# Optimization experiments

Measured on AMD Instinct MI355X. Metric: run time of the kernel, lower is better.

## Reference

```python
import jax, jax.numpy as jnp
import numpy as np

NUM_HEADS = 12


def setup_inputs() -> dict:
    key = jax.random.key(0)
    k1, k2, k3 = jax.random.split(key, 3)
    B, F, P, D = 8, 16, 196, 768
    x = jax.random.normal(k1, (B, F, P, D), dtype=jnp.float32)
    w_qkv = jax.random.normal(k2, (3 * D, D), dtype=jnp.float32) * (D ** -0.5)
    w_proj = jax.random.normal(k3, (D, D), dtype=jnp.float32) * (D ** -0.5)
    b_proj = jnp.zeros((D,), dtype=jnp.float32)
    return {"x": x, "w_qkv": w_qkv, "w_proj": w_proj, "b_proj": b_proj}


def reference(x, w_qkv, w_proj, b_proj):
    B, F, P, D = x.shape
    H = NUM_HEADS
    hd = D // H
    H2 = H // 2
    scale = hd ** -0.5
    N = F * P

    xf = x.reshape(B, N, D)
    qkv = jnp.einsum('bnd,ed->bne', xf, w_qkv)              # (B, N, 3D)
    qkv = qkv.reshape(B, N, 3, H, hd).transpose(2, 0, 3, 1, 4)
    q, k, v = qkv[0], qkv[1], qkv[2]                         # (B, H, N, hd)

    # split heads: first half spatial, second half temporal
    qs, qt = q[:, :H2], q[:, H2:]
    ks, kt = k[:, :H2], k[:, H2:]
    vs, vt = v[:, :H2], v[:, H2:]

    # spatial attention over patches within each frame
    qs = qs.reshape(B * F, H2, P, hd)
    ks = ks.reshape(B * F, H2, P, hd)
    vs = vs.reshape(B * F, H2, P, hd)
    attn_s = jax.nn.softmax(jnp.einsum('nhqd,nhkd->nhqk', qs, ks) * scale, axis=-1)
    ws = jnp.einsum('nhqk,nhkd->nhqd', attn_s, vs)           # (B*F, H2, P, hd)

    # temporal attention: raw row-major reshape, faithful to torch .reshape
    qt = qt.reshape(B * P, H2, F, hd)
    kt = kt.reshape(B * P, H2, F, hd)
    vt = vt.reshape(B * P, H2, F, hd)
    attn_t = jax.nn.softmax(jnp.einsum('mhqd,mhkd->mhqk', qt, kt) * scale, axis=-1)
    wt = jnp.einsum('mhqk,mhkd->mhqd', attn_t, vt)           # (B*P, H2, F, hd)

    ws = ws.reshape(B, H2, N, hd)
    wt = wt.reshape(B, H2, N, hd)
    w = jnp.concatenate([ws, wt], axis=1)                    # (B, H, N, hd)
    w = w.transpose(0, 2, 1, 3).reshape(B, N, D)

    out = jnp.einsum('bnd,ed->bne', w, w_proj) + b_proj
    return out.reshape(B, F, P, D)
```

## Files before the change

### kernel.cpp

```cpp
#include <hip/hip_runtime.h>

#define DEV __device__ __forceinline__

typedef _Float16 half8  __attribute__((ext_vector_type(8)));
typedef _Float16 half4h __attribute__((ext_vector_type(4)));
typedef float    f32x4  __attribute__((ext_vector_type(4)));

static constexpr int Bb = 8;
static constexpr int Ff = 16;
static constexpr int Pp = 196;
static constexpr int Dd = 768;
static constexpr int Hh = 12;
static constexpr int HD = 64;
static constexpr int Nn = 3136;
static constexpr int NC = 392;

#define MFMA(a, b, c) __builtin_amdgcn_mfma_f32_16x16x32_f16(a, b, c, 0, 0, 0)

DEV void gll16(const _Float16* g, _Float16* l) {
  __builtin_amdgcn_global_load_lds(
      (__attribute__((address_space(1))) void*)(g),
      (__attribute__((address_space(3))) void*)(l), 16, 0, 0);
}

DEV void lds_fence() { asm volatile("s_waitcnt lgkmcnt(0)" ::: "memory"); }

__global__ __launch_bounds__(256) void cvt_all(const float* __restrict__ x,
                                               const float* __restrict__ wq,
                                               const float* __restrict__ wp,
                                               _Float16* __restrict__ xh,
                                               _Float16* __restrict__ wqh,
                                               _Float16* __restrict__ wph) {
  const int NX = 4816896, NQ = 442368;
  int i = blockIdx.x * 256 + threadIdx.x;
  const float* s;
  _Float16* d;
  int j;
  if (i < NX) { s = x; d = xh; j = i; }
  else if (i < NX + NQ) { s = wq; d = wqh; j = i - NX; }
  else { s = wp; d = wph; j = i - NX - NQ; }
  f32x4 v = ((const f32x4*)s)[j];
  half4h h;
  h.x = (_Float16)v.x; h.y = (_Float16)v.y;
  h.z = (_Float16)v.z; h.w = (_Float16)v.w;
  ((half4h*)d)[j] = h;
}

__global__ __launch_bounds__(256) void gemm_qkv(const _Float16* __restrict__ X,
                                                const _Float16* __restrict__ W,
                                                _Float16* __restrict__ Q8,
                                                _Float16* __restrict__ K8,
                                                _Float16* __restrict__ V8) {
  __shared__ __align__(16) _Float16 smem[128 * 132];
  _Float16* As = smem;
  _Float16* Bs = smem + 128 * 32;
  const int tid = threadIdx.x;
  const int lane = tid & 63, wid = tid >> 6;
  const int l15 = lane & 15, quad = lane >> 4;
  const int row0 = blockIdx.y * 128;
  const int e0 = blockIdx.x * 128;
  const int wm = (wid >> 1) * 64, wn = (wid & 1) * 64;

  const _Float16* Ag = X + (size_t)row0 * Dd;
  const _Float16* Bg = W + (size_t)e0 * Dd;

  f32x4 acc[4][4];
#pragma unroll
  for (int i = 0; i < 4; ++i)
#pragma unroll
    for (int j = 0; j < 4; ++j) acc[i][j] = (f32x4)0.0f;

  const int c0 = tid, c1 = tid + 256;
  const int r0s = c0 >> 2, o0 = ((c0 & 3) ^ ((r0s >> 1) & 3)) * 8;
  const int r1s = c1 >> 2, o1 = ((c1 & 3) ^ ((r1s >> 1) & 3)) * 8;
  const int csel = ((quad ^ ((l15 >> 1) & 3))) * 8;

  for (int kt = 0; kt < 24; ++kt) {
    const int k0 = kt * 32;
    __syncthreads();
    gll16(Ag + (size_t)r0s * Dd + k0 + o0, As + c0 * 8);
    gll16(Bg + (size_t)r0s * Dd + k0 + o0, Bs + c0 * 8);
    gll16(Ag + (size_t)r1s * Dd + k0 + o1, As + c1 * 8);
    gll16(Bg + (size_t)r1s * Dd + k0 + o1, Bs + c1 * 8);
    __syncthreads();
    half8 af[4], bf[4];
#pragma unroll
    for (int t = 0; t < 4; ++t) {
      af[t] = *(const half8*)(As + (wm + t * 16 + l15) * 32 + csel);
      bf[t] = *(const half8*)(Bs + (wn + t * 16 + l15) * 32 + csel);
    }
#pragma unroll
    for (int i = 0; i < 4; ++i)
#pragma unroll
      for (int j = 0; j < 4; ++j) acc[i][j] = MFMA(af[i], bf[j], acc[i][j]);
  }

  __syncthreads();
  const int tsel = e0 / Dd;
  if (tsel == 2) {
#pragma unroll
    for (int i = 0; i < 4; ++i)
#pragma unroll
      for (int j = 0; j < 4; ++j) {
        const int m = wm + i * 16 + quad * 4;
        const int n = wn + j * 16 + l15;
        half4h hv;
        hv.x = (_Float16)acc[i][j].x; hv.y = (_Float16)acc[i][j].y;
        hv.z = (_Float16)acc[i][j].z; hv.w = (_Float16)acc[i][j].w;
        *(half4h*)(smem + n * 132 + m) = hv;
      }
    __syncthreads();
    for (int c = tid; c < 2048; c += 256) {
      const int ncl = c >> 7, el = c & 127;
      const int e = e0 + el;
      const int h = (e >> 6) % Hh, d = e & 63;
      const int r = row0 + ncl * 8;
      const int b = r / Nn, n = r % Nn;
      const half4h lo = *(const half4h*)(smem + el * 132 + ncl * 8);
      const half4h hi = *(const half4h*)(smem + el * 132 + ncl * 8 + 4);
      half8 v;
#pragma unroll
      for (int z = 0; z < 4; ++z) { v[z] = lo[z]; v[4 + z] = hi[z]; }
      *(half8*)(V8 + (((size_t)(b * Hh + h) * NC + (n >> 3)) * 64 + d) * 8) = v;
    }
  } else {
    _Float16* Ob = (tsel == 0) ? Q8 : K8;
#pragma unroll
    for (int i = 0; i < 4; ++i)
#pragma unroll
      for (int j = 0; j < 4; ++j) {
        const int n = wn + j * 16 + l15;
#pragma unroll
        for (int r = 0; r < 4; ++r) {
          const int m = wm + i * 16 + quad * 4 + r;
          smem[m * 132 + n] = (_Float16)acc[i][j][r];
        }
      }
    __syncthreads();
    for (int c = tid; c < 2048; c += 256) {
      const int ec = c >> 7, m = c & 127;
      const int r = row0 + m;
      const int b = r / Nn, n = r % Nn;
      const int e = e0 + ec * 8;
      const int h = (e >> 6) % Hh, dc = (e >> 3) & 7;
      const half4h lo = *(const half4h*)(smem + m * 132 + ec * 8);
      const half4h hi = *(const half4h*)(smem + m * 132 + ec * 8 + 4);
      half8 v;
#pragma unroll
      for (int z = 0; z < 4; ++z) { v[z] = lo[z]; v[4 + z] = hi[z]; }
      *(half8*)(Ob + (((size_t)(b * Hh + h) * 8 + dc) * Nn + n) * 8) = v;
    }
  }
}

__global__ __launch_bounds__(256) void gemm_proj(const _Float16* __restrict__ Wbuf,
                                                 const _Float16* __restrict__ Wp,
                                                 const float* __restrict__ bias,
                                                 float* __restrict__ Out) {
  __shared__ __align__(16) _Float16 smem[128 * 64];
  _Float16* As = smem;
  _Float16* Bs = smem + 128 * 32;
  const int tid = threadIdx.x;
  const int lane = tid & 63, wid = tid >> 6;
  const int l15 = lane & 15, quad = lane >> 4;
  const int row0 = blockIdx.y * 128;
  const int e0 = blockIdx.x * 128;
  const int wm = (wid >> 1) * 64, wn = (wid & 1) * 64;

  const _Float16* Ag = Wbuf + (size_t)row0 * Dd;
  const _Float16* Bg = Wp + (size_t)e0 * Dd;

  f32x4 acc[4][4];
#pragma unroll
  for (int i = 0; i < 4; ++i)
#pragma unroll
    for (int j = 0; j < 4; ++j) acc[i][j] = (f32x4)0.0f;

  const int c0 = tid, c1 = tid + 256;
  const int r0s = c0 >> 2, o0 = ((c0 & 3) ^ ((r0s >> 1) & 3)) * 8;
  const int r1s = c1 >> 2, o1 = ((c1 & 3) ^ ((r1s >> 1) & 3)) * 8;
  const int csel = ((quad ^ ((l15 >> 1) & 3))) * 8;

  for (int kt = 0; kt < 24; ++kt) {
    const int k0 = kt * 32;
    __syncthreads();
    gll16(Ag + (size_t)r0s * Dd + k0 + o0, As + c0 * 8);
    gll16(Bg + (size_t)r0s * Dd + k0 + o0, Bs + c0 * 8);
    gll16(Ag + (size_t)r1s * Dd + k0 + o1, As + c1 * 8);
    gll16(Bg + (size_t)r1s * Dd + k0 + o1, Bs + c1 * 8);
    __syncthreads();
    half8 af[4], bf[4];
#pragma unroll
    for (int t = 0; t < 4; ++t) {
      af[t] = *(const half8*)(As + (wm + t * 16 + l15) * 32 + csel);
      bf[t] = *(const half8*)(Bs + (wn + t * 16 + l15) * 32 + csel);
    }
#pragma unroll
    for (int i = 0; i < 4; ++i)
#pragma unroll
      for (int j = 0; j < 4; ++j) acc[i][j] = MFMA(af[i], bf[j], acc[i][j]);
  }

#pragma unroll
  for (int j = 0; j < 4; ++j) {
    const int e = e0 + wn + j * 16 + l15;
    const float bj = bias[e];
#pragma unroll
    for (int i = 0; i < 4; ++i) {
      const int rb = row0 + wm + i * 16 + quad * 4;
#pragma unroll
      for (int r = 0; r < 4; ++r)
        Out[(size_t)(rb + r) * Dd + e] = acc[i][j][r] + bj;
    }
  }
}

__global__ __launch_bounds__(256) void attn_spatial(const _Float16* __restrict__ Q8,
                                                    const _Float16* __restrict__ K8,
                                                    const _Float16* __restrict__ V8,
                                                    _Float16* __restrict__ Wbuf) {
  __shared__ __align__(16) _Float16 Vs[64 * 216];
  __shared__ __align__(16) _Float16 Plds[4][16 * 232];
  const int tid = threadIdx.x;
  const int lane = tid & 63, wid = tid >> 6;
  const int l15 = lane & 15, quad = lane >> 4;
  const int gid = blockIdx.x;
  const int h = gid % 6, f = (gid / 6) % Ff, b = gid / 96;
  const size_t bh = (size_t)b * Hh + h;
  const int g0 = f * Pp;
  const int off = g0 & 7;
  const int nc0 = g0 >> 3;
  const _Float16* Qp = Q8 + bh * 8 * (size_t)Nn * 8;
  const _Float16* Kp = K8 + bh * 8 * (size_t)Nn * 8;

  for (int c = tid; c < 26 * 64; c += 256) {
    const int d = c & 63, ncl = c >> 6;
    const half8 v = *(const half8*)(V8 + ((bh * NC + nc0 + ncl) * 64 + d) * 8);
    _Float16* dst = Vs + d * 216 + (8 - off) + ncl * 8;
    half4h lo, hi;
#pragma unroll
    for (int z = 0; z < 4; ++z) { lo[z] = v[z]; hi[z] = v[4 + z]; }
    *(half4h*)dst = lo;
    *(half4h*)(dst + 4) = hi;
  }
  _Float16* Pw = &Plds[wid][0];
  if (quad < 3) {
    half8 z8;
#pragma unroll
    for (int z = 0; z < 8; ++z) z8[z] = (_Float16)0.0f;
    *(half8*)(Pw + l15 * 232 + 208 + quad * 8) = z8;
  }
  __syncthreads();

  half8 h8z;
#pragma unroll
  for (int z = 0; z < 8; ++z) h8z[z] = (_Float16)0.0f;

  for (int it = 0; it < 4; ++it) {
    const int qi = wid + it * 4;
    if (qi > 12) continue;
    const int qr = qi * 16 + l15;
    const int qtok = g0 + (qr < 195 ? qr : 195);
    const half8 bq0 = *(const half8*)(Qp + ((size_t)quad * Nn + qtok) * 8);
    const half8 bq1 = *(const half8*)(Qp + ((size_t)(quad + 4) * Nn + qtok) * 8);

    f32x4 ex[13];
    float rs = 0.0f;
#pragma unroll
    for (int kt = 0; kt < 13; ++kt) {
      const int krr = kt * 16 + l15;
      const int ktok = g0 + (krr < 195 ? krr : 195);
      const half8 ak0 = *(const half8*)(Kp + ((size_t)quad * Nn + ktok) * 8);
      const half8 ak1 = *(const half8*)(Kp + ((size_t)(quad + 4) * Nn + ktok) * 8);
      f32x4 t = (f32x4)0.0f;
      t = MFMA(ak0, bq0, t);
      t = MFMA(ak1, bq1, t);
      f32x4 e;
#pragma unroll
      for (int r = 0; r < 4; ++r) e[r] = __expf(t[r] * 0.125f);
      if (kt == 12 && quad >= 1) e = (f32x4)0.0f;
      ex[kt] = e;
      rs += e[0] + e[1] + e[2] + e[3];
    }
#pragma unroll
    for (int kt = 0; kt < 13; ++kt)
#pragma unroll
      for (int r = 0; r < 4; ++r)
        Pw[l15 * 232 + kt * 16 + quad * 4 + r] = (_Float16)ex[kt][r];
    rs += __shfl_xor(rs, 16);
    rs += __shfl_xor(rs, 32);
    lds_fence();

    f32x4 acc[4];
#pragma unroll
    for (int mt = 0; mt < 4; ++mt) acc[mt] = (f32x4)0.0f;
#pragma unroll
    for (int c = 0; c < 7; ++c) {
      const half8 bp = *(const half8*)(Pw + l15 * 232 + c * 32 + quad * 8);
      const int k0 = c * 32 + quad * 8;
#pragma unroll
      for (int mt = 0; mt < 4; ++mt) {
        const int d = mt * 16 + l15;
        half8 av = h8z;
        if (k0 < 196) av = *(const half8*)(Vs + d * 216 + 8 + k0);
        acc[mt] = MFMA(av, bp, acc[mt]);
      }
    }
    const float inv = 1.0f / rs;
    if (qr < 196) {
      _Float16* base = Wbuf + (size_t)(b * Nn + g0 + qr) * Dd + h * HD;
#pragma unroll
      for (int mt = 0; mt < 4; ++mt) {
        half4h o;
#pragma unroll
        for (int r = 0; r < 4; ++r) o[r] = (_Float16)(acc[mt][r] * inv);
        *(half4h*)(base + mt * 16 + quad * 4) = o;
      }
    }
    __builtin_amdgcn_sched_barrier(0);
  }
}

__global__ __launch_bounds__(256) void attn_temporal(const _Float16* __restrict__ Q8,
                                                     const _Float16* __restrict__ K8,
                                                     const _Float16* __restrict__ V8,
                                                     _Float16* __restrict__ Wbuf) {
  __shared__ __align__(16) _Float16 Plds[4][16 * 40];
  const int tid = threadIdx.x;
  const int lane = tid & 63, wid = tid >> 6;
  const int l15 = lane & 15, quad = lane >> 4;
  const int p = blockIdx.x * 4 + wid;
  const int J0 = p << 4;
  const int b = J0 / 18816;
  const int rem = J0 % 18816;
  const int hh = rem / Nn;
  const int n0 = rem % Nn;
  const size_t bh = (size_t)b * Hh + 6 + hh;
  const _Float16* Qp = Q8 + bh * 8 * (size_t)Nn * 8;
  const _Float16* Kp = K8 + bh * 8 * (size_t)Nn * 8;
  _Float16* Pw = &Plds[wid][0];

  const int tok = n0 + l15;
  const half8 bq0 = *(const half8*)(Qp + ((size_t)quad * Nn + tok) * 8);
  const half8 bq1 = *(const half8*)(Qp + ((size_t)(quad + 4) * Nn + tok) * 8);
  const half8 ak0 = *(const half8*)(Kp + ((size_t)quad * Nn + tok) * 8);
  const half8 ak1 = *(const half8*)(Kp + ((size_t)(quad + 4) * Nn + tok) * 8);
  f32x4 t = (f32x4)0.0f;
  t = MFMA(ak0, bq0, t);
  t = MFMA(ak1, bq1, t);
  f32x4 e;
#pragma unroll
  for (int r = 0; r < 4; ++r) e[r] = __expf(t[r] * 0.125f);
  float rs = e[0] + e[1] + e[2] + e[3];
  rs += __shfl_xor(rs, 16);
  rs += __shfl_xor(rs, 32);

#pragma unroll
  for (int r = 0; r < 4; ++r) Pw[l15 * 40 + quad * 4 + r] = (_Float16)e[r];
  {
    half4h z4;
    z4.x = z4.y = z4.z = z4.w = (_Float16)0.0f;
    *(half4h*)(Pw + l15 * 40 + 16 + quad * 4) = z4;
  }
  lds_fence();

  const half8 bp = *(const half8*)(Pw + l15 * 40 + quad * 8);
  half8 h8z;
#pragma unroll
  for (int z = 0; z < 8; ++z) h8z[z] = (_Float16)0.0f;

  const float inv = 1.0f / rs;
  _Float16* base = Wbuf + (size_t)(b * Nn + n0 + l15) * Dd + (6 + hh) * HD;
#pragma unroll
  for (int mt = 0; mt < 4; ++mt) {
    const int d = mt * 16 + l15;
    half8 av = h8z;
    if (quad < 2)
      av = *(const half8*)(V8 + ((bh * NC + (n0 >> 3) + quad) * 64 + d) * 8);
    f32x4 acc = (f32x4)0.0f;
    acc = MFMA(av, bp, acc);
    half4h o;
#pragma unroll
    for (int r = 0; r < 4; ++r) o[r] = (_Float16)(acc[r] * inv);
    *(half4h*)(base + mt * 16 + quad * 4) = o;
  }
}

extern "C" void kernel_launch(void* const* d_in, const int* in_sizes, int n_in,
                              void* d_out, int out_size, void* d_ws, size_t ws_size,
                              hipStream_t stream) {
  const float* x = (const float*)d_in[0];
  const float* w_qkv = (const float*)d_in[1];
  const float* w_proj = (const float*)d_in[2];
  const float* b_proj = (const float*)d_in[3];
  float* out = (float*)d_out;

  _Float16* Xh = (_Float16*)d_ws;
  _Float16* Q8 = Xh + 19267584;
  _Float16* K8 = Q8 + 19267584;
  _Float16* V8 = K8 + 19267584;
  _Float16* Wqh = V8 + 19267584;
  _Float16* Wph = Wqh + 1769472;

  cvt_all<<<21120, 256, 0, stream>>>(x, w_qkv, w_proj, Xh, Wqh, Wph);
  gemm_qkv<<<dim3(18, 196), 256, 0, stream>>>(Xh, Wqh, Q8, K8, V8);
  attn_spatial<<<768, 256, 0, stream>>>(Q8, K8, V8, Xh);
  attn_temporal<<<2352, 256, 0, stream>>>(Q8, K8, V8, Xh);
  gemm_proj<<<dim3(6, 196), 256, 0, stream>>>(Xh, Wph, b_proj, out);
}
```

Baseline: 367.7 us.

## Rewrite QKV GEMM with 256x256 tiles and triple-buffered async LDS pipeline

The QKV projection GEMM moves from 128x128 tiles with 4 waves and a load/sync/compute loop to 256x256 tiles with 8 waves. It triple-buffers LDS with direct global-to-LDS loads issued two k-steps ahead, split across the two MFMA phases, and uses explicit vmcnt waits, raw barriers and setprio around MFMA bursts. The goal is to hide global load latency and raise arithmetic intensity per block. In exchange it uses more registers and LDS per block, runs fewer blocks (882), and adds an epilogue that writes out in two halves.

```diff
diff --git a/kernel.cpp b/kernel.cpp
--- a/kernel.cpp
+++ b/kernel.cpp
@@ -24,6 +24,7 @@
 }
 
 DEV void lds_fence() { asm volatile("s_waitcnt lgkmcnt(0)" ::: "memory"); }
+#define ASM_BARRIER() asm volatile("s_barrier" ::: "memory")
 
 __global__ __launch_bounds__(256) void cvt_all(const float* __restrict__ x,
                                                const float* __restrict__ wq,
@@ -46,109 +47,154 @@
   ((half4h*)d)[j] = h;
 }
 
-__global__ __launch_bounds__(256) void gemm_qkv(const _Float16* __restrict__ X,
-                                                const _Float16* __restrict__ W,
-                                                _Float16* __restrict__ Q8,
-                                                _Float16* __restrict__ K8,
-                                                _Float16* __restrict__ V8) {
-  __shared__ __align__(16) _Float16 smem[128 * 132];
-  _Float16* As = smem;
-  _Float16* Bs = smem + 128 * 32;
+__global__ __launch_bounds__(512, 2) void gemm_qkv(const _Float16* __restrict__ X,
+                                                   const _Float16* __restrict__ W,
+                                                   _Float16* __restrict__ Q8,
+                                                   _Float16* __restrict__ K8,
+                                                   _Float16* __restrict__ V8) {
+  __shared__ __align__(16) _Float16 smem[3 * 16384];
   const int tid = threadIdx.x;
   const int lane = tid & 63, wid = tid >> 6;
   const int l15 = lane & 15, quad = lane >> 4;
-  const int row0 = blockIdx.y * 128;
-  const int e0 = blockIdx.x * 128;
-  const int wm = (wid >> 1) * 64, wn = (wid & 1) * 64;
+  const int wm = (wid >> 2) * 128, wn = (wid & 3) * 64;
+  const int row0 = blockIdx.y * 256;
+  const int e0 = blockIdx.x * 256;
 
   const _Float16* Ag = X + (size_t)row0 * Dd;
   const _Float16* Bg = W + (size_t)e0 * Dd;
 
-  f32x4 acc[4][4];
-#pragma unroll
-  for (int i = 0; i < 4; ++i)
+  const int c0 = tid, c1 = tid + 512;
+  const int r0 = c0 >> 2, o0 = ((c0 & 3) ^ ((r0 >> 1) & 3)) * 8;
+  const int r1 = c1 >> 2, o1 = ((c1 & 3) ^ ((r1 >> 1) & 3)) * 8;
+  const int csel = (quad ^ ((l15 >> 1) & 3)) * 8;
+
+  f32x4 acc[8][4];
+#pragma unroll
+  for (int i = 0; i < 8; ++i)
 #pragma unroll
     for (int j = 0; j < 4; ++j) acc[i][j] = (f32x4)0.0f;
 
-  const int c0 = tid, c1 = tid + 256;
-  const int r0s = c0 >> 2, o0 = ((c0 & 3) ^ ((r0s >> 1) & 3)) * 8;
-  const int r1s = c1 >> 2, o1 = ((c1 & 3) ^ ((r1s >> 1) & 3)) * 8;
-  const int csel = ((quad ^ ((l15 >> 1) & 3))) * 8;
-
-  for (int kt = 0; kt < 24; ++kt) {
-    const int k0 = kt * 32;
-    __syncthreads();
-    gll16(Ag + (size_t)r0s * Dd + k0 + o0, As + c0 * 8);
-    gll16(Bg + (size_t)r0s * Dd + k0 + o0, Bs + c0 * 8);
-    gll16(Ag + (size_t)r1s * Dd + k0 + o1, As + c1 * 8);
-    gll16(Bg + (size_t)r1s * Dd + k0 + o1, Bs + c1 * 8);
-    __syncthreads();
-    half8 af[4], bf[4];
-#pragma unroll
-    for (int t = 0; t < 4; ++t) {
-      af[t] = *(const half8*)(As + (wm + t * 16 + l15) * 32 + csel);
-      bf[t] = *(const half8*)(Bs + (wn + t * 16 + l15) * 32 + csel);
-    }
+  {
+    _Float16* A0 = smem;
+    _Float16* B0 = smem + 8192;
+    gll16(Ag + (size_t)r0 * Dd + 0 + o0, A0 + c0 * 8);
+    gll16(Ag + (size_t)r1 * Dd + 0 + o1, A0 + c1 * 8);
+    gll16(Bg + (size_t)r0 * Dd + 0 + o0, B0 + c0 * 8);
+    gll16(Bg + (size_t)r1 * Dd + 0 + o1, B0 + c1 * 8);
+    _Float16* A1 = smem + 16384;
+    _Float16* B1 = A1 + 8192;
+    gll16(Ag + (size_t)r0 * Dd + 32 + o0, A1 + c0 * 8);
+    gll16(Ag + (size_t)r1 * Dd + 32 + o1, A1 + c1 * 8);
+    gll16(Bg + (size_t)r0 * Dd + 32 + o0, B1 + c0 * 8);
+    gll16(Bg + (size_t)r1 * Dd + 32 + o1, B1 + c1 * 8);
+  }
+  asm volatile("s_waitcnt vmcnt(4)" ::: "memory");
+  ASM_BARRIER();
+
+  for (int t = 0; t < 24; ++t) {
+    const _Float16* As = smem + (t % 3) * 16384;
+    const _Float16* Bs = As + 8192;
+    const int nb = (t + 2) % 3;
+    const int k0n = (t + 2) * 32;
+    half8 a0[4], bfr[4];
 #pragma unroll
     for (int i = 0; i < 4; ++i)
-#pragma unroll
-      for (int j = 0; j < 4; ++j) acc[i][j] = MFMA(af[i], bf[j], acc[i][j]);
+      a0[i] = *(const half8*)(As + (wm + i * 16 + l15) * 32 + csel);
+#pragma unroll
+    for (int j = 0; j < 4; ++j)
+      bfr[j] = *(const half8*)(Bs + (wn + j * 16 + l15) * 32 + csel);
+    if (t < 22) {
+      _Float16* An = smem + nb * 16384;
+      gll16(Ag + (size_t)r0 * Dd + k0n + o0, An + c0 * 8);
+      gll16(Ag + (size_t)r1 * Dd + k0n + o1, An + c1 * 8);
+    }
+    ASM_BARRIER();
+    __builtin_amdgcn_s_setprio(1);
+#pragma unroll
+    for (int i = 0; i < 4; ++i)
+#pragma unroll
+      for (int j = 0; j < 4; ++j) acc[i][j] = MFMA(a0[i], bfr[j], acc[i][j]);
+    __builtin_amdgcn_s_setprio(0);
+    lds_fence();
+    ASM_BARRIER();
+    half8 a1[4];
+#pragma unroll
+    for (int i = 0; i < 4; ++i)
+      a1[i] = *(const half8*)(As + (wm + 64 + i * 16 + l15) * 32 + csel);
+    if (t < 22) {
+      _Float16* Bn = smem + nb * 16384 + 8192;
+      gll16(Bg + (size_t)r0 * Dd + k0n + o0, Bn + c0 * 8);
+      gll16(Bg + (size_t)r1 * Dd + k0n + o1, Bn + c1 * 8);
+    }
+    if (t < 22) asm volatile("s_waitcnt vmcnt(4)" ::: "memory");
+    else if (t == 22) asm volatile("s_waitcnt vmcnt(0)" ::: "memory");
+    ASM_BARRIER();
+    __builtin_amdgcn_s_setprio(1);
+#pragma unroll
+    for (int i = 0; i < 4; ++i)
+#pragma unroll
+      for (int j = 0; j < 4; ++j) acc[4 + i][j] = MFMA(a1[i], bfr[j], acc[4 + i][j]);
+    __builtin_amdgcn_s_setprio(0);
+    lds_fence();
+    ASM_BARRIER();
   }
 
   __syncthreads();
   const int tsel = e0 / Dd;
+  const int eb = e0 - tsel * Dd;
   if (tsel == 2) {
-#pragma unroll
-    for (int i = 0; i < 4; ++i)
-#pragma unroll
-      for (int j = 0; j < 4; ++j) {
-        const int m = wm + i * 16 + quad * 4;
-        const int n = wn + j * 16 + l15;
-        half4h hv;
-        hv.x = (_Float16)acc[i][j].x; hv.y = (_Float16)acc[i][j].y;
-        hv.z = (_Float16)acc[i][j].z; hv.w = (_Float16)acc[i][j].w;
-        *(half4h*)(smem + n * 132 + m) = hv;
-      }
-    __syncthreads();
-    for (int c = tid; c < 2048; c += 256) {
-      const int ncl = c >> 7, el = c & 127;
-      const int e = e0 + el;
-      const int h = (e >> 6) % Hh, d = e & 63;
-      const int r = row0 + ncl * 8;
-      const int b = r / Nn, n = r % Nn;
-      const half4h lo = *(const half4h*)(smem + el * 132 + ncl * 8);
-      const half4h hi = *(const half4h*)(smem + el * 132 + ncl * 8 + 4);
-      half8 v;
-#pragma unroll
-      for (int z = 0; z < 4; ++z) { v[z] = lo[z]; v[4 + z] = hi[z]; }
-      *(half8*)(V8 + (((size_t)(b * Hh + h) * NC + (n >> 3)) * 64 + d) * 8) = v;
+    for (int hf = 0; hf < 2; ++hf) {
+      if ((wid >> 2) == hf) {
+#pragma unroll
+        for (int i = 0; i < 8; ++i)
+#pragma unroll
+          for (int j = 0; j < 4; ++j) {
+            half4h hv;
+#pragma unroll
+            for (int r = 0; r < 4; ++r) hv[r] = (_Float16)acc[i][j][r];
+            *(half4h*)(smem + (wn + j * 16 + l15) * 136 + i * 16 + quad * 4) = hv;
+          }
+      }
+      __syncthreads();
+#pragma unroll
+      for (int z = 0; z < 8; ++z) {
+        const int c = tid + z * 512;
+        const int e = c >> 4, mc = c & 15;
+        const half8 v = *(const half8*)(smem + e * 136 + mc * 8);
+        const int rg = row0 + hf * 128 + mc * 8;
+        const int b = rg / Nn, n = rg % Nn;
+        const int eg = eb + e;
+        const int hh = eg >> 6, d = eg & 63;
+        *(half8*)(V8 + (((size_t)(b * Hh + hh) * NC + (n >> 3)) * 64 + d) * 8) = v;
+      }
+      __syncthreads();
     }
   } else {
     _Float16* Ob = (tsel == 0) ? Q8 : K8;
-#pragma unroll
-    for (int i = 0; i < 4; ++i)
-#pragma unroll
-      for (int j = 0; j < 4; ++j) {
-        const int n = wn + j * 16 + l15;
-#pragma unroll
-        for (int r = 0; r < 4; ++r) {
-          const int m = wm + i * 16 + quad * 4 + r;
-          smem[m * 132 + n] = (_Float16)acc[i][j][r];
-        }
-      }
-    __syncthreads();
-    for (int c = tid; c < 2048; c += 256) {
-      const int ec = c >> 7, m = c & 127;
-      const int r = row0 + m;
-      const int b = r / Nn, n = r % Nn;
-      const int e = e0 + ec * 8;
-      const int h = (e >> 6) % Hh, dc = (e >> 3) & 7;
-      const half4h lo = *(const half4h*)(smem + m * 132 + ec * 8);
-      const half4h hi = *(const half4h*)(smem + m * 132 + ec * 8 + 4);
-      half8 v;
-#pragma unroll
-      for (int z = 0; z < 4; ++z) { v[z] = lo[z]; v[4 + z] = hi[z]; }
-      *(half8*)(Ob + (((size_t)(b * Hh + h) * 8 + dc) * Nn + n) * 8) = v;
+    for (int hf = 0; hf < 2; ++hf) {
+      if ((wid >> 2) == hf) {
+#pragma unroll
+        for (int i = 0; i < 8; ++i)
+#pragma unroll
+          for (int j = 0; j < 4; ++j)
+#pragma unroll
+            for (int r = 0; r < 4; ++r)
+              smem[(i * 16 + quad * 4 + r) * 264 + wn + j * 16 + l15] =
+                  (_Float16)acc[i][j][r];
+      }
+      __syncthreads();
+#pragma unroll
+      for (int z = 0; z < 8; ++z) {
+        const int c = tid + z * 512;
+        const int m = c >> 5, ec = c & 31;
+        const half8 v = *(const half8*)(smem + m * 264 + ec * 8);
+        const int rg = row0 + hf * 128 + m;
+        const int b = rg / Nn, n = rg % Nn;
+        const int eg = eb + ec * 8;
+        const int hh = eg >> 6, dc = (eg >> 3) & 7;
+        *(half8*)(Ob + (((size_t)(b * Hh + hh) * 8 + dc) * Nn + n) * 8) = v;
+      }
+      __syncthreads();
     }
   }
 }
@@ -403,7 +449,7 @@
   _Float16* Wph = Wqh + 1769472;
 
   cvt_all<<<21120, 256, 0, stream>>>(x, w_qkv, w_proj, Xh, Wqh, Wph);
-  gemm_qkv<<<dim3(18, 196), 256, 0, stream>>>(Xh, Wqh, Q8, K8, V8);
+  gemm_qkv<<<dim3(9, 98), 512, 0, stream>>>(Xh, Wqh, Q8, K8, V8);
   attn_spatial<<<768, 256, 0, stream>>>(Q8, K8, V8, Xh);
   attn_temporal<<<2352, 256, 0, stream>>>(Q8, K8, V8, Xh);
   gemm_proj<<<dim3(6, 196), 256, 0, stream>>>(Xh, Wph, b_proj, out);
```

Result: slower. 412.8 us (+12.3%).
